# Performance work log

Hardware: AMD Instinct MI355X
Metric: run time of the kernel (lower is better)

The kernel has to match this reference:

```python
import jax, jax.numpy as jnp
import numpy as np

B, S_SRC, S_TGT = 32, 64, 1024
D, H, DFF, LE, LD, V = 128, 8, 512, 6, 6, 64


def _pe(S, d):
    # PyTorch-style sinusoidal positional encoding, shape [S, d]
    pos = np.arange(S, dtype=np.float32)[:, None]
    div = np.exp(np.arange(0, d, 2, dtype=np.float32) * (-np.log(10000.0) / d))
    pe = np.zeros((S, d), dtype=np.float32)
    pe[:, 0::2] = np.sin(pos * div)
    pe[:, 1::2] = np.cos(pos * div)
    return jnp.asarray(pe)


def _ln(x, g, b, eps=1e-5):
    m = x.mean(-1, keepdims=True)
    v = ((x - m) ** 2).mean(-1, keepdims=True)
    return (x - m) / jnp.sqrt(v + eps) * g + b


def _mha(q_in, k_in, v_in, Wqkv, bqkv, Wo, bo):
    d = q_in.shape[-1]
    dh = d // H
    def proj(x, W, b):
        return (x @ W.T + b).reshape(x.shape[0], x.shape[1], H, dh)
    q = proj(q_in, Wqkv[:d], bqkv[:d])
    k = proj(k_in, Wqkv[d:2 * d], bqkv[d:2 * d])
    v = proj(v_in, Wqkv[2 * d:], bqkv[2 * d:])
    scores = jnp.einsum('bqhd,bkhd->bhqk', q, k) * (1.0 / np.sqrt(dh))
    a = jax.nn.softmax(scores, axis=-1)
    o = jnp.einsum('bhqk,bkhd->bqhd', a, v).reshape(q_in.shape[0], q_in.shape[1], d)
    return o @ Wo.T + bo


def _ffn(x, W1, b1, W2, b2):
    return jax.nn.relu(x @ W1.T + b1) @ W2.T + b2


def reference(src, tgt, emb,
              enc_qkv_w, enc_qkv_b, enc_out_w, enc_out_b,
              enc_ln1_g, enc_ln1_b, enc_ff1_w, enc_ff1_b,
              enc_ff2_w, enc_ff2_b, enc_ln2_g, enc_ln2_b,
              enc_norm_g, enc_norm_b,
              dec_sa_qkv_w, dec_sa_qkv_b, dec_sa_out_w, dec_sa_out_b,
              dec_ln1_g, dec_ln1_b,
              dec_ca_qkv_w, dec_ca_qkv_b, dec_ca_out_w, dec_ca_out_b,
              dec_ln2_g, dec_ln2_b,
              dec_ff1_w, dec_ff1_b, dec_ff2_w, dec_ff2_b,
              dec_ln3_g, dec_ln3_b, dec_norm_g, dec_norm_b,
              fc_w, fc_b):
    # src: [B, S_SRC] int tokens (occupation config); tgt: [B, S_TGT, D] (zeros in the original)
    s = emb[src] * np.sqrt(float(D)) + _pe(src.shape[1], D)
    t = tgt + _pe(tgt.shape[1], D)
    # encoder (post-norm, ReLU, dropout=0 in eval)
    for i in range(LE):
        s = _ln(s + _mha(s, s, s, enc_qkv_w[i], enc_qkv_b[i], enc_out_w[i], enc_out_b[i]),
                enc_ln1_g[i], enc_ln1_b[i])
        s = _ln(s + _ffn(s, enc_ff1_w[i], enc_ff1_b[i], enc_ff2_w[i], enc_ff2_b[i]),
                enc_ln2_g[i], enc_ln2_b[i])
    mem = _ln(s, enc_norm_g, enc_norm_b)
    # decoder
    for i in range(LD):
        t = _ln(t + _mha(t, t, t, dec_sa_qkv_w[i], dec_sa_qkv_b[i], dec_sa_out_w[i], dec_sa_out_b[i]),
                dec_ln1_g[i], dec_ln1_b[i])
        t = _ln(t + _mha(t, mem, mem, dec_ca_qkv_w[i], dec_ca_qkv_b[i], dec_ca_out_w[i], dec_ca_out_b[i]),
                dec_ln2_g[i], dec_ln2_b[i])
        t = _ln(t + _ffn(t, dec_ff1_w[i], dec_ff1_b[i], dec_ff2_w[i], dec_ff2_b[i]),
                dec_ln3_g[i], dec_ln3_b[i])
    t = _ln(t, dec_norm_g, dec_norm_b)
    return t @ fc_w.T + fc_b  # [B, S_TGT, 1] transformer correction to TN params


def setup_inputs():
    ks = iter(jax.random.split(jax.random.key(0), 64))
    def nrm(shape, scale=0.02):
        return jax.random.normal(next(ks), shape, dtype=jnp.float32) * scale
    inp = {
        'src': jax.random.randint(next(ks), (B, S_SRC), 0, V),
        'tgt': jnp.zeros((B, S_TGT, D), jnp.float32),
        'emb': nrm((V, D), 1.0),
        'enc_qkv_w': nrm((LE, 3 * D, D)), 'enc_qkv_b': jnp.zeros((LE, 3 * D)),
        'enc_out_w': nrm((LE, D, D)), 'enc_out_b': jnp.zeros((LE, D)),
        'enc_ln1_g': jnp.ones((LE, D)), 'enc_ln1_b': jnp.zeros((LE, D)),
        'enc_ff1_w': nrm((LE, DFF, D)), 'enc_ff1_b': jnp.zeros((LE, DFF)),
        'enc_ff2_w': nrm((LE, D, DFF)), 'enc_ff2_b': jnp.zeros((LE, D)),
        'enc_ln2_g': jnp.ones((LE, D)), 'enc_ln2_b': jnp.zeros((LE, D)),
        'enc_norm_g': jnp.ones((D,)), 'enc_norm_b': jnp.zeros((D,)),
        'dec_sa_qkv_w': nrm((LD, 3 * D, D)), 'dec_sa_qkv_b': jnp.zeros((LD, 3 * D)),
        'dec_sa_out_w': nrm((LD, D, D)), 'dec_sa_out_b': jnp.zeros((LD, D)),
        'dec_ln1_g': jnp.ones((LD, D)), 'dec_ln1_b': jnp.zeros((LD, D)),
        'dec_ca_qkv_w': nrm((LD, 3 * D, D)), 'dec_ca_qkv_b': jnp.zeros((LD, 3 * D)),
        'dec_ca_out_w': nrm((LD, D, D)), 'dec_ca_out_b': jnp.zeros((LD, D)),
        'dec_ln2_g': jnp.ones((LD, D)), 'dec_ln2_b': jnp.zeros((LD, D)),
        'dec_ff1_w': nrm((LD, DFF, D)), 'dec_ff1_b': jnp.zeros((LD, DFF)),
        'dec_ff2_w': nrm((LD, D, DFF)), 'dec_ff2_b': jnp.zeros((LD, D)),
        'dec_ln3_g': jnp.ones((LD, D)), 'dec_ln3_b': jnp.zeros((LD, D)),
        'dec_norm_g': jnp.ones((D,)), 'dec_norm_b': jnp.zeros((D,)),
        'fc_w': nrm((1, D)), 'fc_b': jnp.zeros((1,)),
    }
    return inp
```

## Files before the change

### kernel.cpp

```cpp
#include <hip/hip_runtime.h>
#include <hip/hip_bf16.h>
#include <stdint.h>

#define NH 8

typedef uint16_t u16;
typedef uint32_t u32;
typedef __attribute__((ext_vector_type(2))) u32 u32x2;
typedef __attribute__((ext_vector_type(8))) short s8b;
typedef __attribute__((ext_vector_type(4))) float f32x4;
typedef __attribute__((ext_vector_type(16))) float f32x16;

#if __has_builtin(__builtin_amdgcn_exp2f)
#define EXPS(x) __builtin_amdgcn_exp2f(x)
#define QSCALE 0.36067376022224085f
#else
#define EXPS(x) __expf(x)
#define QSCALE 0.25f
#endif

__device__ __forceinline__ u16 f2b(float f) {
    u32 u = __builtin_bit_cast(u32, f);
    u = (u + 0x7fffu + ((u >> 16) & 1u)) >> 16;
    return (u16)u;
}
__device__ __forceinline__ float b2f(u16 u) {
    return __builtin_bit_cast(float, (u32)u << 16);
}
__device__ __forceinline__ u32 pkbf(float a, float b) {
    u32 ua = __builtin_bit_cast(u32, a) + 0x8000u;
    u32 ub = __builtin_bit_cast(u32, b) + 0x8000u;
    return __builtin_amdgcn_perm(ub, ua, 0x07060302);
}

__device__ __forceinline__ float pe_val(int pos, int d) {
    int j = d >> 1;
    float div = expf((float)j * -0.14391156831212787f);
    float ang = (float)pos * div;
    return (d & 1) ? cosf(ang) : sinf(ang);
}

__global__ void embed_kernel(const int* __restrict__ src, const float* __restrict__ emb,
                             u16* __restrict__ Sb) {
    int idx = blockIdx.x * 256 + threadIdx.x;
    int d = idx & 127;
    int n = idx >> 7;
    int i = n & 63;
    int tok = src[n];
    Sb[idx] = f2b(emb[tok * 128 + d] * 11.313708498984761f + pe_val(i, d));
}

__global__ void addpe_kernel(const float* __restrict__ tgt, u16* __restrict__ Tb) {
    int idx = blockIdx.x * 256 + threadIdx.x;
    int d = idx & 127;
    int n = idx >> 7;
    int i = n & 1023;
    Tb[idx] = f2b(tgt[idx] + pe_val(i, d));
}

struct CvtJobs { const float* src[10]; u16* dst[10]; int n[10]; };
__global__ void cvt_kernel(CvtJobs jb) {
    int e = blockIdx.y;
    int i = blockIdx.x * 256 + threadIdx.x;
    if (i < jb.n[e]) jb.dst[e][i] = f2b(jb.src[e][i]);
}

template <int RELU>
__global__ __launch_bounds__(256) void gemm_mfma(
    const u16* __restrict__ A, const u16* __restrict__ W,
    const float* __restrict__ bias, u16* __restrict__ C,
    int M, int N, int K, float qscale, int qcols,
    u16* __restrict__ vt, int vcol0, int sshift, int smask, int skv) {
    __shared__ __align__(16) u16 As[128 * 56];
    __shared__ __align__(16) u16 Bs[128 * 56];
    int tid = threadIdx.x;
    int lane = tid & 63, w = tid >> 6;
    int quad = lane >> 4, l15 = lane & 15;
    int m0 = blockIdx.y * 128, n0 = blockIdx.x * 128;
    int wm = (w & 1) * 64, wn = (w >> 1) * 64;
    int srow = tid >> 1, skof = (tid & 1) * 16;

    f32x4 acc[4][4];
#pragma unroll
    for (int i = 0; i < 4; i++)
#pragma unroll
        for (int j = 0; j < 4; j++)
#pragma unroll
            for (int r = 0; r < 4; r++) acc[i][j][r] = 0.f;

    for (int k0 = 0; k0 < K; k0 += 32) {
        const u16* ga = A + (size_t)(m0 + srow) * K + k0 + skof;
        const u16* gw = W + (size_t)(n0 + srow) * K + k0 + skof;
        s8b a0 = *(const s8b*)ga, a1 = *(const s8b*)(ga + 8);
        s8b w0 = *(const s8b*)gw, w1 = *(const s8b*)(gw + 8);
        __syncthreads();
        *(s8b*)(As + srow * 56 + skof) = a0;
        *(s8b*)(As + srow * 56 + skof + 8) = a1;
        *(s8b*)(Bs + srow * 56 + skof) = w0;
        *(s8b*)(Bs + srow * 56 + skof + 8) = w1;
        __syncthreads();
        s8b af[4], bfr[4];
#pragma unroll
        for (int i = 0; i < 4; i++) af[i] = *(const s8b*)(As + (wm + 16 * i + l15) * 56 + quad * 8);
#pragma unroll
        for (int j = 0; j < 4; j++) bfr[j] = *(const s8b*)(Bs + (wn + 16 * j + l15) * 56 + quad * 8);
#pragma unroll
        for (int i = 0; i < 4; i++)
#pragma unroll
            for (int j = 0; j < 4; j++)
                acc[i][j] = __builtin_amdgcn_mfma_f32_16x16x32_bf16(af[i], bfr[j], acc[i][j], 0, 0, 0);
    }

    if (vt && n0 == vcol0) {
#pragma unroll
        for (int j = 0; j < 4; j++) {
            int lc = wn + 16 * j + l15;
            int h = lc >> 4, n = lc & 15;
            float bv = bias[vcol0 + lc];
#pragma unroll
            for (int i = 0; i < 4; i++) {
                int row = m0 + wm + 16 * i + quad * 4;
                int b = row >> sshift, tok = row & smask;
                u32 lo = pkbf(acc[i][j][0] + bv, acc[i][j][1] + bv);
                u32 hi = pkbf(acc[i][j][2] + bv, acc[i][j][3] + bv);
                u32* p = (u32*)(vt + ((size_t)((b * 8 + h) * 16 + n)) * skv + tok);
                p[0] = lo; p[1] = hi;
            }
        }
        return;
    }
#pragma unroll
    for (int j = 0; j < 4; j++) {
        int col = n0 + wn + 16 * j + l15;
        float bv = bias[col];
        float sc = (col < qcols) ? qscale : 1.f;
#pragma unroll
        for (int i = 0; i < 4; i++) {
            int rbase = m0 + wm + 16 * i + quad * 4;
#pragma unroll
            for (int r = 0; r < 4; r++) {
                float v = (acc[i][j][r] + bv) * sc;
                if (RELU) v = fmaxf(v, 0.f);
                C[(size_t)(rbase + r) * N + col] = f2b(v);
            }
        }
    }
}

__global__ __launch_bounds__(256) void gemm_ln(
    const u16* __restrict__ A, const u16* __restrict__ W,
    const float* __restrict__ bias, const u16* __restrict__ X,
    const float* __restrict__ g, const float* __restrict__ bta,
    u16* __restrict__ Yb, int M, int K) {
    __shared__ __align__(16) u16 As[128 * 56];
    __shared__ __align__(16) u16 Bs[128 * 56];
    __shared__ float redS[128][2], redQ[128][2];
    int tid = threadIdx.x;
    int lane = tid & 63, w = tid >> 6;
    int quad = lane >> 4, l15 = lane & 15;
    int m0 = blockIdx.x * 128;
    int wm = (w & 1) * 64, wn = (w >> 1) * 64;
    int srow = tid >> 1, skof = (tid & 1) * 16;

    f32x4 acc[4][4];
#pragma unroll
    for (int i = 0; i < 4; i++)
#pragma unroll
        for (int j = 0; j < 4; j++)
#pragma unroll
            for (int r = 0; r < 4; r++) acc[i][j][r] = 0.f;

    for (int k0 = 0; k0 < K; k0 += 32) {
        const u16* ga = A + (size_t)(m0 + srow) * K + k0 + skof;
        const u16* gw = W + (size_t)srow * K + k0 + skof;
        s8b a0 = *(const s8b*)ga, a1 = *(const s8b*)(ga + 8);
        s8b w0 = *(const s8b*)gw, w1 = *(const s8b*)(gw + 8);
        __syncthreads();
        *(s8b*)(As + srow * 56 + skof) = a0;
        *(s8b*)(As + srow * 56 + skof + 8) = a1;
        *(s8b*)(Bs + srow * 56 + skof) = w0;
        *(s8b*)(Bs + srow * 56 + skof + 8) = w1;
        __syncthreads();
        s8b af[4], bfr[4];
#pragma unroll
        for (int i = 0; i < 4; i++) af[i] = *(const s8b*)(As + (wm + 16 * i + l15) * 56 + quad * 8);
#pragma unroll
        for (int j = 0; j < 4; j++) bfr[j] = *(const s8b*)(Bs + (wn + 16 * j + l15) * 56 + quad * 8);
#pragma unroll
        for (int i = 0; i < 4; i++)
#pragma unroll
            for (int j = 0; j < 4; j++)
                acc[i][j] = __builtin_amdgcn_mfma_f32_16x16x32_bf16(af[i], bfr[j], acc[i][j], 0, 0, 0);
    }

    float s_[4][4], q_[4][4];
#pragma unroll
    for (int i = 0; i < 4; i++)
#pragma unroll
        for (int r = 0; r < 4; r++) {
            int row = m0 + wm + 16 * i + quad * 4 + r;
            float s = 0.f, q = 0.f;
#pragma unroll
            for (int j = 0; j < 4; j++) {
                int col = wn + 16 * j + l15;
                float x = acc[i][j][r] + bias[col] + b2f(X[(size_t)row * 128 + col]);
                acc[i][j][r] = x;
                s += x; q += x * x;
            }
#pragma unroll
            for (int off = 1; off < 16; off <<= 1) {
                s += __shfl_xor(s, off);
                q += __shfl_xor(q, off);
            }
            s_[i][r] = s; q_[i][r] = q;
        }
    if (l15 == 0) {
#pragma unroll
        for (int i = 0; i < 4; i++)
#pragma unroll
            for (int r = 0; r < 4; r++) {
                int lrow = wm + 16 * i + quad * 4 + r;
                redS[lrow][wn >> 6] = s_[i][r];
                redQ[lrow][wn >> 6] = q_[i][r];
            }
    }
    __syncthreads();
#pragma unroll
    for (int i = 0; i < 4; i++)
#pragma unroll
        for (int r = 0; r < 4; r++) {
            int lrow = wm + 16 * i + quad * 4 + r;
            int row = m0 + lrow;
            float S2 = redS[lrow][0] + redS[lrow][1];
            float Q2 = redQ[lrow][0] + redQ[lrow][1];
            float mean = S2 * (1.f / 128.f);
            float var = Q2 * (1.f / 128.f) - mean * mean;
            float rstd = rsqrtf(var + 1e-5f);
#pragma unroll
            for (int j = 0; j < 4; j++) {
                int col = wn + 16 * j + l15;
                float y = (acc[i][j][r] - mean) * rstd * g[col] + bta[col];
                Yb[(size_t)row * 128 + col] = f2b(y);
            }
        }
}

template <int WAVES>
__global__ __launch_bounds__(WAVES * 64) void attn3(
    const u16* __restrict__ Qb, int qstride,
    const u16* __restrict__ Kb, int kstride, int koff,
    const u16* __restrict__ VT,
    u16* __restrict__ O, int SQ, int SKV) {
    __shared__ __align__(16) u32 Ps[WAVES][32 * 20];
    int tid = threadIdx.x;
    int lane = tid & 63, w = tid >> 6;
    int quad = lane >> 4, l15 = lane & 15, l31 = lane & 31, half = lane >> 5;
    int nqc = SQ / (WAVES * 32);
    int bid = blockIdx.x;
    int qc = bid % nqc;
    int h = (bid / nqc) % NH;
    int b = bid / (nqc * NH);
    int q0 = qc * WAVES * 32 + w * 32;

    const u16* qp = Qb + (size_t)(b * SQ + q0 + l31) * qstride + h * 16 + half * 8;
    s8b qf = *(const s8b*)qp;
    s8b ones;
#pragma unroll
    for (int j = 0; j < 8; j++) ones[j] = (short)0x3F80;

    const u16* vtb = VT + ((size_t)(b * NH + h) * 16 + l15) * SKV + quad * 8;
    const u16* kp = Kb + (size_t)(b * SKV + l31) * kstride + koff + h * 16 + half * 8;
    size_t kadv = (size_t)32 * kstride;

    f32x4 O0, O1, L0, L1;
#pragma unroll
    for (int r = 0; r < 4; r++) { O0[r] = 0.f; O1[r] = 0.f; L0[r] = 0.f; L1[r] = 0.f; }

    u32* pw = Ps[w];
#pragma unroll 2
    for (int j0 = 0; j0 < SKV; j0 += 32) {
        s8b kf = *(const s8b*)kp;
        kp += kadv;
        s8b vb = *(const s8b*)(vtb + j0);
        f32x16 S;
#pragma unroll
        for (int r = 0; r < 16; r++) S[r] = 0.f;
        S = __builtin_amdgcn_mfma_f32_32x32x16_bf16(kf, qf, S, 0, 0, 0);
#pragma unroll
        for (int g = 0; g < 4; g++) {
            float p0 = EXPS(S[4 * g + 0]);
            float p1 = EXPS(S[4 * g + 1]);
            float p2 = EXPS(S[4 * g + 2]);
            float p3 = EXPS(S[4 * g + 3]);
            u32x2 pk;
            pk[0] = pkbf(p0, p1);
            pk[1] = pkbf(p2, p3);
            *(u32x2*)(pw + l31 * 20 + 2 * half + 4 * g) = pk;
        }
        __builtin_amdgcn_wave_barrier();
        s8b pa0 = *(const s8b*)(pw + l15 * 20 + quad * 4);
        s8b pa1 = *(const s8b*)(pw + (16 + l15) * 20 + quad * 4);
        O0 = __builtin_amdgcn_mfma_f32_16x16x32_bf16(pa0, vb, O0, 0, 0, 0);
        O1 = __builtin_amdgcn_mfma_f32_16x16x32_bf16(pa1, vb, O1, 0, 0, 0);
        L0 = __builtin_amdgcn_mfma_f32_16x16x32_bf16(pa0, ones, L0, 0, 0, 0);
        L1 = __builtin_amdgcn_mfma_f32_16x16x32_bf16(pa1, ones, L1, 0, 0, 0);
    }
#pragma unroll
    for (int r = 0; r < 4; r++) {
        int q = b * SQ + q0 + quad * 4 + r;
        O[(size_t)q * 128 + h * 16 + l15] = f2b(O0[r] / L0[r]);
        O[(size_t)(q + 16) * 128 + h * 16 + l15] = f2b(O1[r] / L1[r]);
    }
}

__global__ void ln_bf(const u16* __restrict__ X,
                      const float* __restrict__ g, const float* __restrict__ bta,
                      float* __restrict__ Yf, u16* __restrict__ Yb) {
    int r = blockIdx.x;
    int lane = threadIdx.x;
    size_t base = (size_t)r * 128;
    float x0 = b2f(X[base + lane]), x1 = b2f(X[base + lane + 64]);
    float s = x0 + x1;
    for (int off = 32; off; off >>= 1) s += __shfl_xor(s, off);
    float mean = s * (1.f / 128.f);
    float d0 = x0 - mean, d1 = x1 - mean;
    float vs = d0 * d0 + d1 * d1;
    for (int off = 32; off; off >>= 1) vs += __shfl_xor(vs, off);
    float rstd = rsqrtf(vs * (1.f / 128.f) + 1e-5f);
    float y0 = d0 * rstd * g[lane] + bta[lane];
    float y1 = d1 * rstd * g[lane + 64] + bta[lane + 64];
    if (Yf) { Yf[base + lane] = y0; Yf[base + lane + 64] = y1; }
    if (Yb) { Yb[base + lane] = f2b(y0); Yb[base + lane + 64] = f2b(y1); }
}

__global__ void fc_kernel(const float* __restrict__ X, const float* __restrict__ w,
                          const float* __restrict__ b, float* __restrict__ out) {
    int r = blockIdx.x;
    int lane = threadIdx.x;
    size_t base = (size_t)r * 128;
    float s = X[base + lane] * w[lane] + X[base + lane + 64] * w[lane + 64];
    for (int off = 32; off; off >>= 1) s += __shfl_xor(s, off);
    if (lane == 0) out[r] = s + b[0];
}

static inline void gemm_b(const u16* A, const u16* W, const float* bias, u16* C,
                          int M, int N, int K, hipStream_t st, int qcols = 0,
                          u16* vt = nullptr, int vcol0 = 0, int sshift = 0, int skv = 0) {
    hipLaunchKernelGGL((gemm_mfma<0>), dim3(N / 128, M / 128), dim3(256), 0, st,
                       A, W, bias, C, M, N, K, QSCALE, qcols, vt, vcol0, sshift,
                       (1 << sshift) - 1, skv);
}
static inline void gemm_br(const u16* A, const u16* W, const float* bias, u16* C,
                           int M, int N, int K, hipStream_t st) {
    hipLaunchKernelGGL((gemm_mfma<1>), dim3(N / 128, M / 128), dim3(256), 0, st,
                       A, W, bias, C, M, N, K, 1.f, 0, (u16*)nullptr, 0, 0, 0, 0);
}
static inline void gemmln(const u16* A, const u16* W, const float* bias,
                          const u16* X, const float* g, const float* bta,
                          u16* Yb, int M, int K, hipStream_t st) {
    hipLaunchKernelGGL(gemm_ln, dim3(M / 128), dim3(256), 0, st,
                       A, W, bias, X, g, bta, Yb, M, K);
}

extern "C" void kernel_launch(void* const* d_in, const int* in_sizes, int n_in,
                              void* d_out, int out_size, void* d_ws, size_t ws_size,
                              hipStream_t stream) {
    const int B = 32, SSRC = 64, STGT = 1024, D = 128, DFF_ = 512, LE = 6, LD = 6;

    const int*   src = (const int*)d_in[0];
    const float* tgt = (const float*)d_in[1];
    const float* emb = (const float*)d_in[2];
    const float* enc_qkv_w = (const float*)d_in[3];
    const float* enc_qkv_b = (const float*)d_in[4];
    const float* enc_out_w = (const float*)d_in[5];
    const float* enc_out_b = (const float*)d_in[6];
    const float* enc_ln1_g = (const float*)d_in[7];
    const float* enc_ln1_b = (const float*)d_in[8];
    const float* enc_ff1_w = (const float*)d_in[9];
    const float* enc_ff1_b = (const float*)d_in[10];
    const float* enc_ff2_w = (const float*)d_in[11];
    const float* enc_ff2_b = (const float*)d_in[12];
    const float* enc_ln2_g = (const float*)d_in[13];
    const float* enc_ln2_b = (const float*)d_in[14];
    const float* enc_norm_g = (const float*)d_in[15];
    const float* enc_norm_b = (const float*)d_in[16];
    const float* dec_sa_qkv_w = (const float*)d_in[17];
    const float* dec_sa_qkv_b = (const float*)d_in[18];
    const float* dec_sa_out_w = (const float*)d_in[19];
    const float* dec_sa_out_b = (const float*)d_in[20];
    const float* dec_ln1_g = (const float*)d_in[21];
    const float* dec_ln1_b = (const float*)d_in[22];
    const float* dec_ca_qkv_w = (const float*)d_in[23];
    const float* dec_ca_qkv_b = (const float*)d_in[24];
    const float* dec_ca_out_w = (const float*)d_in[25];
    const float* dec_ca_out_b = (const float*)d_in[26];
    const float* dec_ln2_g = (const float*)d_in[27];
    const float* dec_ln2_b = (const float*)d_in[28];
    const float* dec_ff1_w = (const float*)d_in[29];
    const float* dec_ff1_b = (const float*)d_in[30];
    const float* dec_ff2_w = (const float*)d_in[31];
    const float* dec_ff2_b = (const float*)d_in[32];
    const float* dec_ln3_g = (const float*)d_in[33];
    const float* dec_ln3_b = (const float*)d_in[34];
    const float* dec_norm_g = (const float*)d_in[35];
    const float* dec_norm_b = (const float*)d_in[36];
    const float* fc_w = (const float*)d_in[37];
    const float* fc_b = (const float*)d_in[38];

    const int NT = B * STGT;
    const int NS = B * SSRC;

    u16* t_bf    = (u16*)d_ws;
    u16* s_bf    = t_bf + (size_t)NT * D;
    u16* mem_bf  = s_bf + (size_t)NS * D;
    u16* qkv_bf  = mem_bf + (size_t)NS * D;
    u16* attno_bf = qkv_bf + (size_t)NT * DFF_;
    u16* ckv_bf  = attno_bf + (size_t)NT * D;
    u16* vt      = ckv_bf + (size_t)NS * 2 * D;
    u16* wa      = vt + (size_t)B * NH * 16 * STGT + 16 * STGT;

    u16* w_enc_qkv = wa;                          int n_enc_qkv = LE * 3 * D * D;
    u16* w_enc_out = w_enc_qkv + n_enc_qkv;       int n_enc_out = LE * D * D;
    u16* w_enc_ff1 = w_enc_out + n_enc_out;       int n_enc_ff1 = LE * DFF_ * D;
    u16* w_enc_ff2 = w_enc_ff1 + n_enc_ff1;       int n_enc_ff2 = LE * D * DFF_;
    u16* w_sa_qkv  = w_enc_ff2 + n_enc_ff2;       int n_sa_qkv = LD * 3 * D * D;
    u16* w_sa_out  = w_sa_qkv + n_sa_qkv;         int n_sa_out = LD * D * D;
    u16* w_ca_qkv  = w_sa_out + n_sa_out;         int n_ca_qkv = LD * 3 * D * D;
    u16* w_ca_out  = w_ca_qkv + n_ca_qkv;         int n_ca_out = LD * D * D;
    u16* w_ff1     = w_ca_out + n_ca_out;         int n_ff1 = LD * DFF_ * D;
    u16* w_ff2     = w_ff1 + n_ff1;               int n_ff2 = LD * D * DFF_;

    float* scf = (float*)qkv_bf;

    CvtJobs jb;
    jb.src[0] = enc_qkv_w;    jb.dst[0] = w_enc_qkv; jb.n[0] = n_enc_qkv;
    jb.src[1] = enc_out_w;    jb.dst[1] = w_enc_out; jb.n[1] = n_enc_out;
    jb.src[2] = enc_ff1_w;    jb.dst[2] = w_enc_ff1; jb.n[2] = n_enc_ff1;
    jb.src[3] = enc_ff2_w;    jb.dst[3] = w_enc_ff2; jb.n[3] = n_enc_ff2;
    jb.src[4] = dec_sa_qkv_w; jb.dst[4] = w_sa_qkv;  jb.n[4] = n_sa_qkv;
    jb.src[5] = dec_sa_out_w; jb.dst[5] = w_sa_out;  jb.n[5] = n_sa_out;
    jb.src[6] = dec_ca_qkv_w; jb.dst[6] = w_ca_qkv;  jb.n[6] = n_ca_qkv;
    jb.src[7] = dec_ca_out_w; jb.dst[7] = w_ca_out;  jb.n[7] = n_ca_out;
    jb.src[8] = dec_ff1_w;    jb.dst[8] = w_ff1;     jb.n[8] = n_ff1;
    jb.src[9] = dec_ff2_w;    jb.dst[9] = w_ff2;     jb.n[9] = n_ff2;
    int maxn = n_enc_ff1;
    hipLaunchKernelGGL(cvt_kernel, dim3((maxn + 255) / 256, 10), dim3(256), 0, stream, jb);

    hipLaunchKernelGGL(embed_kernel, dim3(NS * D / 256), dim3(256), 0, stream, src, emb, s_bf);

    for (int i = 0; i < LE; i++) {
        gemm_b(s_bf, w_enc_qkv + (size_t)i * 3 * D * D, enc_qkv_b + (size_t)i * 3 * D,
               qkv_bf, NS, 3 * D, D, stream, 128, vt, 256, 6, SSRC);
        hipLaunchKernelGGL((attn3<2>), dim3(B * NH), dim3(128), 0, stream,
                           qkv_bf, 3 * D, qkv_bf, 3 * D, D, vt, attno_bf, SSRC, SSRC);
        gemmln(attno_bf, w_enc_out + (size_t)i * D * D, enc_out_b + (size_t)i * D,
               s_bf, enc_ln1_g + (size_t)i * D, enc_ln1_b + (size_t)i * D, s_bf, NS, D, stream);
        gemm_br(s_bf, w_enc_ff1 + (size_t)i * DFF_ * D, enc_ff1_b + (size_t)i * DFF_,
                qkv_bf, NS, DFF_, D, stream);
        gemmln(qkv_bf, w_enc_ff2 + (size_t)i * D * DFF_, enc_ff2_b + (size_t)i * D,
               s_bf, enc_ln2_g + (size_t)i * D, enc_ln2_b + (size_t)i * D, s_bf, NS, DFF_, stream);
    }
    hipLaunchKernelGGL(ln_bf, dim3(NS), dim3(64), 0, stream,
                       s_bf, enc_norm_g, enc_norm_b, (float*)nullptr, mem_bf);

    hipLaunchKernelGGL(addpe_kernel, dim3(NT * D / 256), dim3(256), 0, stream, tgt, t_bf);

    for (int i = 0; i < LD; i++) {
        gemm_b(t_bf, w_sa_qkv + (size_t)i * 3 * D * D, dec_sa_qkv_b + (size_t)i * 3 * D,
               qkv_bf, NT, 3 * D, D, stream, 128, vt, 256, 10, STGT);
        hipLaunchKernelGGL((attn3<4>), dim3(B * NH * (STGT / 128)), dim3(256), 0, stream,
                           qkv_bf, 3 * D, qkv_bf, 3 * D, D, vt, attno_bf, STGT, STGT);
        gemmln(attno_bf, w_sa_out + (size_t)i * D * D, dec_sa_out_b + (size_t)i * D,
               t_bf, dec_ln1_g + (size_t)i * D, dec_ln1_b + (size_t)i * D, t_bf, NT, D, stream);

        gemm_b(t_bf, w_ca_qkv + (size_t)i * 3 * D * D, dec_ca_qkv_b + (size_t)i * 3 * D,
               qkv_bf, NT, D, D, stream, 128);
        gemm_b(mem_bf, w_ca_qkv + (size_t)i * 3 * D * D + (size_t)D * D,
               dec_ca_qkv_b + (size_t)i * 3 * D + D, ckv_bf, NS, 2 * D, D, stream,
               0, vt, 128, 6, SSRC);
        hipLaunchKernelGGL((attn3<4>), dim3(B * NH * (STGT / 128)), dim3(256), 0, stream,
                           qkv_bf, D, ckv_bf, 2 * D, 0, vt, attno_bf, STGT, SSRC);
        gemmln(attno_bf, w_ca_out + (size_t)i * D * D, dec_ca_out_b + (size_t)i * D,
               t_bf, dec_ln2_g + (size_t)i * D, dec_ln2_b + (size_t)i * D, t_bf, NT, D, stream);

        gemm_br(t_bf, w_ff1 + (size_t)i * DFF_ * D, dec_ff1_b + (size_t)i * DFF_,
                qkv_bf, NT, DFF_, D, stream);
        gemmln(qkv_bf, w_ff2 + (size_t)i * D * DFF_, dec_ff2_b + (size_t)i * D,
               t_bf, dec_ln3_g + (size_t)i * D, dec_ln3_b + (size_t)i * D, t_bf, NT, DFF_, stream);
    }

    hipLaunchKernelGGL(ln_bf, dim3(NT), dim3(64), 0, stream,
                       t_bf, dec_norm_g, dec_norm_b, scf, (u16*)nullptr);
    hipLaunchKernelGGL(fc_kernel, dim3(NT), dim3(64), 0, stream,
                       scf, fc_w, fc_b, (float*)d_out);
}
```

Baseline: 1.451 ms.

## Prefetch next GEMM k-tile into registers and fuse final LayerNorm with FC

Both GEMM kernels now issue the global loads for the next 32-wide k-slice right after the shared-memory barrier, so memory latency overlaps the MFMA work on the current slice (register double buffering). The final decoder LayerNorm and the output projection are merged into one kernel, which drops a launch and the fp32 round trip through scratch memory. The attention loop also reuses a hoisted zero accumulator. Keeping the prefetched tile live raises register pressure.

```diff
diff --git a/kernel.cpp b/kernel.cpp
--- a/kernel.cpp
+++ b/kernel.cpp
@@ -88,17 +88,22 @@
 #pragma unroll
             for (int r = 0; r < 4; r++) acc[i][j][r] = 0.f;
 
+    const u16* ga = A + (size_t)(m0 + srow) * K + skof;
+    const u16* gw = W + (size_t)(n0 + srow) * K + skof;
+    s8b a0 = *(const s8b*)ga, a1 = *(const s8b*)(ga + 8);
+    s8b w0 = *(const s8b*)gw, w1 = *(const s8b*)(gw + 8);
+
     for (int k0 = 0; k0 < K; k0 += 32) {
-        const u16* ga = A + (size_t)(m0 + srow) * K + k0 + skof;
-        const u16* gw = W + (size_t)(n0 + srow) * K + k0 + skof;
-        s8b a0 = *(const s8b*)ga, a1 = *(const s8b*)(ga + 8);
-        s8b w0 = *(const s8b*)gw, w1 = *(const s8b*)(gw + 8);
         __syncthreads();
         *(s8b*)(As + srow * 56 + skof) = a0;
         *(s8b*)(As + srow * 56 + skof + 8) = a1;
         *(s8b*)(Bs + srow * 56 + skof) = w0;
         *(s8b*)(Bs + srow * 56 + skof + 8) = w1;
         __syncthreads();
+        if (k0 + 32 < K) {
+            a0 = *(const s8b*)(ga + k0 + 32); a1 = *(const s8b*)(ga + k0 + 40);
+            w0 = *(const s8b*)(gw + k0 + 32); w1 = *(const s8b*)(gw + k0 + 40);
+        }
         s8b af[4], bfr[4];
 #pragma unroll
         for (int i = 0; i < 4; i++) af[i] = *(const s8b*)(As + (wm + 16 * i + l15) * 56 + quad * 8);
@@ -170,17 +175,22 @@
 #pragma unroll
             for (int r = 0; r < 4; r++) acc[i][j][r] = 0.f;
 
+    const u16* ga = A + (size_t)(m0 + srow) * K + skof;
+    const u16* gw = W + (size_t)srow * K + skof;
+    s8b a0 = *(const s8b*)ga, a1 = *(const s8b*)(ga + 8);
+    s8b w0 = *(const s8b*)gw, w1 = *(const s8b*)(gw + 8);
+
     for (int k0 = 0; k0 < K; k0 += 32) {
-        const u16* ga = A + (size_t)(m0 + srow) * K + k0 + skof;
-        const u16* gw = W + (size_t)srow * K + k0 + skof;
-        s8b a0 = *(const s8b*)ga, a1 = *(const s8b*)(ga + 8);
-        s8b w0 = *(const s8b*)gw, w1 = *(const s8b*)(gw + 8);
         __syncthreads();
         *(s8b*)(As + srow * 56 + skof) = a0;
         *(s8b*)(As + srow * 56 + skof + 8) = a1;
         *(s8b*)(Bs + srow * 56 + skof) = w0;
         *(s8b*)(Bs + srow * 56 + skof + 8) = w1;
         __syncthreads();
+        if (k0 + 32 < K) {
+            a0 = *(const s8b*)(ga + k0 + 32); a1 = *(const s8b*)(ga + k0 + 40);
+            w0 = *(const s8b*)(gw + k0 + 32); w1 = *(const s8b*)(gw + k0 + 40);
+        }
         s8b af[4], bfr[4];
 #pragma unroll
         for (int i = 0; i < 4; i++) af[i] = *(const s8b*)(As + (wm + 16 * i + l15) * 56 + quad * 8);
@@ -275,6 +285,9 @@
     f32x4 O0, O1, L0, L1;
 #pragma unroll
     for (int r = 0; r < 4; r++) { O0[r] = 0.f; O1[r] = 0.f; L0[r] = 0.f; L1[r] = 0.f; }
+    f32x16 z16;
+#pragma unroll
+    for (int r = 0; r < 16; r++) z16[r] = 0.f;
 
     u32* pw = Ps[w];
 #pragma unroll 2
@@ -282,10 +295,7 @@
         s8b kf = *(const s8b*)kp;
         kp += kadv;
         s8b vb = *(const s8b*)(vtb + j0);
-        f32x16 S;
-#pragma unroll
-        for (int r = 0; r < 16; r++) S[r] = 0.f;
-        S = __builtin_amdgcn_mfma_f32_32x32x16_bf16(kf, qf, S, 0, 0, 0);
+        f32x16 S = __builtin_amdgcn_mfma_f32_32x32x16_bf16(kf, qf, z16, 0, 0, 0);
 #pragma unroll
         for (int g = 0; g < 4; g++) {
             float p0 = EXPS(S[4 * g + 0]);
@@ -315,7 +325,26 @@
 
 __global__ void ln_bf(const u16* __restrict__ X,
                       const float* __restrict__ g, const float* __restrict__ bta,
-                      float* __restrict__ Yf, u16* __restrict__ Yb) {
+                      u16* __restrict__ Yb) {
+    int r = blockIdx.x;
+    int lane = threadIdx.x;
+    size_t base = (size_t)r * 128;
+    float x0 = b2f(X[base + lane]), x1 = b2f(X[base + lane + 64]);
+    float s = x0 + x1;
+    for (int off = 32; off; off >>= 1) s += __shfl_xor(s, off);
+    float mean = s * (1.f / 128.f);
+    float d0 = x0 - mean, d1 = x1 - mean;
+    float vs = d0 * d0 + d1 * d1;
+    for (int off = 32; off; off >>= 1) vs += __shfl_xor(vs, off);
+    float rstd = rsqrtf(vs * (1.f / 128.f) + 1e-5f);
+    Yb[base + lane] = f2b(d0 * rstd * g[lane] + bta[lane]);
+    Yb[base + lane + 64] = f2b(d1 * rstd * g[lane + 64] + bta[lane + 64]);
+}
+
+__global__ void ln_fc(const u16* __restrict__ X,
+                      const float* __restrict__ g, const float* __restrict__ bta,
+                      const float* __restrict__ w, const float* __restrict__ bb,
+                      float* __restrict__ out) {
     int r = blockIdx.x;
     int lane = threadIdx.x;
     size_t base = (size_t)r * 128;
@@ -329,18 +358,9 @@
     float rstd = rsqrtf(vs * (1.f / 128.f) + 1e-5f);
     float y0 = d0 * rstd * g[lane] + bta[lane];
     float y1 = d1 * rstd * g[lane + 64] + bta[lane + 64];
-    if (Yf) { Yf[base + lane] = y0; Yf[base + lane + 64] = y1; }
-    if (Yb) { Yb[base + lane] = f2b(y0); Yb[base + lane + 64] = f2b(y1); }
-}
-
-__global__ void fc_kernel(const float* __restrict__ X, const float* __restrict__ w,
-                          const float* __restrict__ b, float* __restrict__ out) {
-    int r = blockIdx.x;
-    int lane = threadIdx.x;
-    size_t base = (size_t)r * 128;
-    float s = X[base + lane] * w[lane] + X[base + lane + 64] * w[lane + 64];
-    for (int off = 32; off; off >>= 1) s += __shfl_xor(s, off);
-    if (lane == 0) out[r] = s + b[0];
+    float acc = y0 * w[lane] + y1 * w[lane + 64];
+    for (int off = 32; off; off >>= 1) acc += __shfl_xor(acc, off);
+    if (lane == 0) out[r] = acc + bb[0];
 }
 
 static inline void gemm_b(const u16* A, const u16* W, const float* bias, u16* C,
@@ -430,8 +450,6 @@
     u16* w_ff1     = w_ca_out + n_ca_out;         int n_ff1 = LD * DFF_ * D;
     u16* w_ff2     = w_ff1 + n_ff1;               int n_ff2 = LD * D * DFF_;
 
-    float* scf = (float*)qkv_bf;
-
     CvtJobs jb;
     jb.src[0] = enc_qkv_w;    jb.dst[0] = w_enc_qkv; jb.n[0] = n_enc_qkv;
     jb.src[1] = enc_out_w;    jb.dst[1] = w_enc_out; jb.n[1] = n_enc_out;
@@ -461,7 +479,7 @@
                s_bf, enc_ln2_g + (size_t)i * D, enc_ln2_b + (size_t)i * D, s_bf, NS, DFF_, stream);
     }
     hipLaunchKernelGGL(ln_bf, dim3(NS), dim3(64), 0, stream,
-                       s_bf, enc_norm_g, enc_norm_b, (float*)nullptr, mem_bf);
+                       s_bf, enc_norm_g, enc_norm_b, mem_bf);
 
     hipLaunchKernelGGL(addpe_kernel, dim3(NT * D / 256), dim3(256), 0, stream, tgt, t_bf);
 
@@ -489,8 +507,6 @@
                t_bf, dec_ln3_g + (size_t)i * D, dec_ln3_b + (size_t)i * D, t_bf, NT, DFF_, stream);
     }
 
-    hipLaunchKernelGGL(ln_bf, dim3(NT), dim3(64), 0, stream,
-                       t_bf, dec_norm_g, dec_norm_b, scf, (u16*)nullptr);
-    hipLaunchKernelGGL(fc_kernel, dim3(NT), dim3(64), 0, stream,
-                       scf, fc_w, fc_b, (float*)d_out);
-}
+    hipLaunchKernelGGL(ln_fc, dim3(NT), dim3(64), 0, stream,
+                       t_bf, dec_norm_g, dec_norm_b, fc_w, fc_b, (float*)d_out);
+}
```

After: 1.363 ms. 1.06x faster.
